# Kernel optimization log

Hardware: AMD Instinct MI355X
Metric: run time of the kernel (lower is better)

The kernel has to match this reference:

```python
import jax, jax.numpy as jnp
import numpy as np
from math import pi

N = 20000        # nodes
E = 640000       # edges (avg degree 32)
H = 128          # hidden_channels = num_filters
NB = 3           # num_bond_features
NGS = 50 - NB    # gaussians in smearing (num_gaussians - num_bond_features)
CUT = 10.0       # cutoff
L = 3            # num_interactions
B = 16           # graphs in batch
LOG2 = 0.6931471805599453


def ssp(x):
    # ShiftedSoftplus
    return jax.nn.softplus(x) - LOG2


def setup_inputs() -> dict:
    key = jax.random.key(0)
    ks = jax.random.split(key, 20)
    s = 0.05
    inp = {
        "z": jax.random.randint(ks[0], (N,), 0, 100),
        "pos": jax.random.uniform(ks[1], (N, 3), jnp.float32),
        "batch": jnp.sort(jax.random.randint(ks[2], (N,), 0, B)),
        "edge_index": jax.random.randint(ks[3], (2, E), 0, N),
        "edge_attr": jax.random.uniform(ks[4], (E, NB), jnp.float32),
        # parameters (stacked over L interaction blocks where per-layer)
        "emb": jax.random.normal(ks[5], (100, H), jnp.float32) * s,
        "mlp_w1": jax.random.normal(ks[6], (L, NB + NGS, H), jnp.float32) * s,
        "mlp_b1": jnp.zeros((L, H), jnp.float32),
        "mlp_w2": jax.random.normal(ks[7], (L, H, H), jnp.float32) * s,
        "mlp_b2": jnp.zeros((L, H), jnp.float32),
        "cf1_w": jax.random.normal(ks[8], (L, H, H), jnp.float32) * s,   # lin1, no bias
        "cf2_w": jax.random.normal(ks[9], (L, H, H), jnp.float32) * s,
        "cf2_b": jnp.zeros((L, H), jnp.float32),
        "lin_w": jax.random.normal(ks[10], (L, H, H), jnp.float32) * s,
        "lin_b": jnp.zeros((L, H), jnp.float32),
        "out1_w": jax.random.normal(ks[11], (H, H // 2), jnp.float32) * s,
        "out1_b": jnp.zeros((H // 2,), jnp.float32),
        "out2_w": jax.random.normal(ks[12], (H // 2, 1), jnp.float32) * s,
        "out2_b": jnp.zeros((1,), jnp.float32),
    }
    return inp


def reference(z, pos, batch, edge_index, edge_attr, emb,
              mlp_w1, mlp_b1, mlp_w2, mlp_b2,
              cf1_w, cf2_w, cf2_b, lin_w, lin_b,
              out1_w, out1_b, out2_w, out2_b):
    row, col = edge_index[0], edge_index[1]  # source j, target i
    h = emb[z]                               # [N,H] embedding_e(z)
    # edge_weight = ||pos[row] - pos[col]||
    ew = jnp.linalg.norm(pos[row] - pos[col], axis=-1)  # [E]
    # GaussianSmearing(0, cutoff, NGS)
    offset = jnp.linspace(0.0, CUT, NGS, dtype=jnp.float32)
    coeff = -0.5 / (offset[1] - offset[0]) ** 2
    gs = jnp.exp(coeff * (ew[:, None] - offset[None, :]) ** 2)  # [E,NGS]
    ea = jnp.concatenate([edge_attr, gs], axis=1)  # [E,50]
    # cosine cutoff weight
    C = 0.5 * (jnp.cos(ew * pi / CUT) + 1.0)       # [E]
    for l in range(L):
        # filter MLP on edge features
        W = ssp(ea @ mlp_w1[l] + mlp_b1[l]) @ mlp_w2[l] + mlp_b2[l]  # [E,H]
        W = W * C[:, None]
        xh = h @ cf1_w[l]                    # lin1 (no bias) [N,H]
        msg = xh[row] * W                    # gather-mul [E,H]
        agg = jax.ops.segment_sum(msg, col, num_segments=N)  # scatter-add [N,H]
        xc = agg @ cf2_w[l] + cf2_b[l]       # lin2
        xc = ssp(xc)
        xc = xc @ lin_w[l] + lin_b[l]        # block output lin
        h = h + xc                           # residual
    h = ssp(h @ out1_w + out1_b)             # [N,H/2]
    per_node = h @ out2_w + out2_b           # [N,1]
    out = jax.ops.segment_sum(per_node, batch, num_segments=B)  # readout 'add' -> [B,1]
    return out
```

## Files before the change

### kernel.cpp

```cpp
#include <hip/hip_runtime.h>
#include <hip/hip_bf16.h>

typedef __attribute__((ext_vector_type(8))) short bfrag;
typedef __attribute__((ext_vector_type(4))) float f32x4;

__device__ __forceinline__ float ssp_f(float x) {
    return fmaxf(x, 0.f) + __logf(1.f + __expf(-fabsf(x))) - 0.6931471805599453f;
}

__device__ __forceinline__ unsigned short f2b(float x) {
    __hip_bfloat16 h = __float2bfloat16(x);
    return *(unsigned short*)&h;
}

__global__ void sniff_kernel(const unsigned int* __restrict__ raw, int* __restrict__ flag)
{
    __shared__ int cnt[256];
    const int t = threadIdx.x;
    unsigned int w = raw[t];
    unsigned int e = (w >> 7) & 0xFFu;
    cnt[t] = (e >= 100u && e <= 135u) ? 1 : 0;
    __syncthreads();
    for (int s = 128; s > 0; s >>= 1) {
        if (t < s) cnt[t] += cnt[t + s];
        __syncthreads();
    }
    if (t == 0) *flag = (cnt[0] >= 160) ? 1 : 0;
}

__global__ void sniff_int_kernel(const unsigned int* __restrict__ z, int* __restrict__ iflag)
{
    __shared__ int cnt[128];
    const int t = threadIdx.x;
    cnt[t] = (z[2 * t + 1] == 0u) ? 1 : 0;
    __syncthreads();
    for (int s = 64; s > 0; s >>= 1) {
        if (t < s) cnt[t] += cnt[t + s];
        __syncthreads();
    }
    if (t == 0) *iflag = (cnt[0] >= 126) ? 1 : 0;
}

__global__ __launch_bounds__(256) void convert_kernel(
    const void* __restrict__ src, float* __restrict__ dst, int n,
    const int* __restrict__ flag)
{
    int i = blockIdx.x * 256 + threadIdx.x;
    if (i >= n) return;
    if (*flag) dst[i] = __bfloat162float(((const __hip_bfloat16*)src)[i]);
    else       dst[i] = ((const float*)src)[i];
}

__global__ __launch_bounds__(256) void convert_int_kernel(
    const void* __restrict__ src, int* __restrict__ dst, int n,
    const int* __restrict__ iflag)
{
    int i = blockIdx.x * 256 + threadIdx.x;
    if (i >= n) return;
    if (*iflag) dst[i] = (int)(((const long long*)src)[i]);
    else        dst[i] = ((const int*)src)[i];
}

__global__ __launch_bounds__(256) void embed_kernel(
    const int* __restrict__ z, const float* __restrict__ embf,
    float* __restrict__ h, int NH)
{
    int idx = blockIdx.x * 256 + threadIdx.x;
    if (idx >= NH) return;
    h[idx] = embf[z[idx >> 7] * 128 + (idx & 127)];
}

__global__ __launch_bounds__(256) void zero_int_kernel(int* p, int n)
{
    int i = blockIdx.x * 256 + threadIdx.x;
    if (i < n) p[i] = 0;
}

__global__ __launch_bounds__(256) void hist_kernel(const int* __restrict__ col,
                                                   int* __restrict__ count, int E)
{
    int e = blockIdx.x * 256 + threadIdx.x;
    if (e < E) atomicAdd(&count[col[e]], 1);
}

__global__ __launch_bounds__(256) void scan_kernel(const int* __restrict__ count,
                                                   int* __restrict__ rowptr,
                                                   int* __restrict__ next, int N)
{
    __shared__ int part[256];
    const int t = threadIdx.x;
    const int chunk = (N + 255) / 256;
    const int lo = t * chunk, hi = min(lo + chunk, N);
    int s = 0;
    for (int i = lo; i < hi; ++i) s += count[i];
    part[t] = s;
    __syncthreads();
    if (t == 0) {
        int run = 0;
        for (int i = 0; i < 256; ++i) { int v = part[i]; part[i] = run; run += v; }
        rowptr[N] = run;
    }
    __syncthreads();
    int run = part[t];
    for (int i = lo; i < hi; ++i) {
        rowptr[i] = run; next[i] = run;
        run += count[i];
    }
}

__global__ __launch_bounds__(256) void slot_kernel(const int* __restrict__ col,
                                                   int* __restrict__ next,
                                                   int* __restrict__ slot, int E)
{
    int e = blockIdx.x * 256 + threadIdx.x;
    if (e < E) slot[e] = atomicAdd(&next[col[e]], 1);
}

__global__ __launch_bounds__(256) void perm_kernel(const int* __restrict__ slot,
                                                   int* __restrict__ perm, int E)
{
    int e = blockIdx.x * 256 + threadIdx.x;
    if (e < E) perm[slot[e]] = e;
}

__global__ __launch_bounds__(256) void prep_edges_kernel(
    const float* __restrict__ posf, const int* __restrict__ row,
    const int* __restrict__ col, const float* __restrict__ eattrf,
    const int* __restrict__ perm,
    int* __restrict__ rowS, int* __restrict__ colS,
    float* __restrict__ CS, float* __restrict__ ewS,
    unsigned short* __restrict__ eaS, int E, int NB)
{
    int p = blockIdx.x * 256 + threadIdx.x;
    if (p >= E) return;
    const int e = perm[p];
    const int r = row[e], c = col[e];
    float dx = posf[r*3+0] - posf[c*3+0];
    float dy = posf[r*3+1] - posf[c*3+1];
    float dz = posf[r*3+2] - posf[c*3+2];
    float ew = sqrtf(dx*dx + dy*dy + dz*dz);
    rowS[p] = r; colS[p] = c; ewS[p] = ew;
    CS[p] = 0.5f * (cosf(ew * 0.3141592653589793f) + 1.0f);
    unsigned short* o = eaS + (long)p * 4;
    for (int q = 0; q < 4; ++q)
        o[q] = (q < NB) ? f2b(eattrf[(long)e * NB + q]) : (unsigned short)0;
}

__global__ __launch_bounds__(256) void wtrans_kernel(
    const float* __restrict__ src, unsigned short* __restrict__ dst,
    int K, int Kpad, int N)
{
    int idx = blockIdx.x * 256 + threadIdx.x;
    if (idx >= N * Kpad) return;
    int n = idx / Kpad, k = idx - n * Kpad;
    dst[idx] = (k < K) ? f2b(src[k * N + n]) : (unsigned short)0;
}

template<int MODE>
__global__ __launch_bounds__(256) void node_gemm_tiled(
    const float* __restrict__ in, const float* __restrict__ W,
    const float* __restrict__ bias, float* __restrict__ out, int N)
{
    __shared__ float in_s[32][128];
    const int t = threadIdx.x;
    const long n0 = (long)blockIdx.x * 32;
    for (int i = t; i < 32 * 128; i += 256) {
        long n = n0 + (i >> 7);
        in_s[i >> 7][i & 127] = (n < N) ? in[n * 128 + (i & 127)] : 0.f;
    }
    __syncthreads();
    const int j = t & 31, sub = t >> 5;
    const int c4 = j * 4, rb = sub * 4;
    float acc[4][4];
    float4 bv = make_float4(0.f, 0.f, 0.f, 0.f);
    if (MODE != 0) bv = *(const float4*)(bias + c4);
    #pragma unroll
    for (int i = 0; i < 4; ++i) { acc[i][0]=bv.x; acc[i][1]=bv.y; acc[i][2]=bv.z; acc[i][3]=bv.w; }
    #pragma unroll 4
    for (int k = 0; k < 128; ++k) {
        const float4 wv = *(const float4*)(W + k * 128 + c4);
        #pragma unroll
        for (int i = 0; i < 4; ++i) {
            const float a = in_s[rb + i][k];
            acc[i][0] += a * wv.x; acc[i][1] += a * wv.y;
            acc[i][2] += a * wv.z; acc[i][3] += a * wv.w;
        }
    }
    #pragma unroll
    for (int i = 0; i < 4; ++i) {
        long n = n0 + rb + i;
        if (n >= N) continue;
        float4 o;
        if (MODE == 1) {
            o.x = ssp_f(acc[i][0]); o.y = ssp_f(acc[i][1]);
            o.z = ssp_f(acc[i][2]); o.w = ssp_f(acc[i][3]);
        } else {
            o.x = acc[i][0]; o.y = acc[i][1]; o.z = acc[i][2]; o.w = acc[i][3];
        }
        if (MODE == 2) {
            float4 p = *(const float4*)(out + n * 128 + c4);
            o.x += p.x; o.y += p.y; o.z += p.z; o.w += p.w;
        }
        *(float4*)(out + n * 128 + c4) = o;
    }
}

__global__ __launch_bounds__(256) void edge_mfma(
    const int* __restrict__ rowS, const int* __restrict__ colS,
    const float* __restrict__ CS, const float* __restrict__ ewS,
    const unsigned short* __restrict__ eaS,
    const unsigned short* __restrict__ w1t, const float* __restrict__ b1,
    const unsigned short* __restrict__ w2t, const float* __restrict__ b2,
    const float* __restrict__ xh, float* __restrict__ agg,
    int E, int NB, int F50, float delta, float coeff)
{
    __shared__ __align__(16) short ea_b[32][64];
    __shared__ __align__(16) short t_b[32][128];
    __shared__ float runbuf[32][136];
    __shared__ int   row_s[32];
    __shared__ int   col_s[32];
    __shared__ float C_s[32];
    __shared__ float ew_s[32];
    __shared__ int   runcol_s[32];
    __shared__ int   runstart_s[33];
    __shared__ int   nruns_s;

    const int t = threadIdx.x;
    const long p0 = (long)blockIdx.x * 32;

    if (t < 32) {
        long p = p0 + t; if (p >= E) p = E - 1;
        row_s[t] = rowS[p];
        col_s[t] = colS[p];
        C_s[t]   = (p0 + t < E) ? CS[p] : 0.f;
        ew_s[t]  = ewS[p];
    }
    __syncthreads();
    if (t == 0) {
        int nr = 0;
        for (int i = 0; i < 32; ++i) {
            if (i == 0 || col_s[i] != col_s[i - 1]) {
                runcol_s[nr] = col_s[i];
                runstart_s[nr] = i;
                ++nr;
            }
        }
        runstart_s[nr] = 32;
        nruns_s = nr;
    }
    for (int i = t; i < 32 * 64; i += 256) {
        const int e = i >> 6, k = i & 63;
        long p = p0 + e; if (p >= E) p = E - 1;
        unsigned short v;
        if (k < NB)        v = eaS[p * 4 + k];
        else if (k < F50) {
            float d = ew_s[e] - (float)(k - NB) * delta;
            v = f2b(__expf(coeff * d * d));
        } else             v = 0;
        ea_b[e][k] = (short)v;
    }
    __syncthreads();

    const int lane = t & 63;
    const int w    = t >> 6;
    const int colL = lane & 15;
    const int quad = lane >> 4;
    const int m0   = (w & 1) * 16;

    {
        f32x4 acc[4];
        #pragma unroll
        for (int tt = 0; tt < 4; ++tt) acc[tt] = (f32x4){0.f, 0.f, 0.f, 0.f};
        #pragma unroll
        for (int ks = 0; ks < 2; ++ks) {
            const bfrag a = *(const bfrag*)&ea_b[m0 + colL][ks * 32 + quad * 8];
            #pragma unroll
            for (int tt = 0; tt < 4; ++tt) {
                const int n0 = ((w >> 1) * 4 + tt) * 16;
                const bfrag b = *(const bfrag*)&w1t[(long)(n0 + colL) * 64 + ks * 32 + quad * 8];
                acc[tt] = __builtin_amdgcn_mfma_f32_16x16x32_bf16(a, b, acc[tt], 0, 0, 0);
            }
        }
        #pragma unroll
        for (int tt = 0; tt < 4; ++tt) {
            const int n0 = ((w >> 1) * 4 + tt) * 16;
            const float bcol = b1[n0 + colL];
            #pragma unroll
            for (int reg = 0; reg < 4; ++reg) {
                float v = ssp_f(acc[tt][reg] + bcol);
                t_b[m0 + quad * 4 + reg][n0 + colL] = (short)f2b(v);
            }
        }
    }
    __syncthreads();

    {
        f32x4 acc[4];
        #pragma unroll
        for (int tt = 0; tt < 4; ++tt) acc[tt] = (f32x4){0.f, 0.f, 0.f, 0.f};
        #pragma unroll
        for (int ks = 0; ks < 4; ++ks) {
            const bfrag a = *(const bfrag*)&t_b[m0 + colL][ks * 32 + quad * 8];
            #pragma unroll
            for (int tt = 0; tt < 4; ++tt) {
                const int n0 = ((w >> 1) * 4 + tt) * 16;
                const bfrag b = *(const bfrag*)&w2t[(long)(n0 + colL) * 128 + ks * 32 + quad * 8];
                acc[tt] = __builtin_amdgcn_mfma_f32_16x16x32_bf16(a, b, acc[tt], 0, 0, 0);
            }
        }
        const int ebase = m0 + quad * 4;
        #pragma unroll
        for (int tt = 0; tt < 4; ++tt) {
            const int n0 = ((w >> 1) * 4 + tt) * 16;
            const int cg = n0 + colL;
            const float bcol = b2[cg];
            #pragma unroll
            for (int reg = 0; reg < 4; ++reg) {
                const int e = ebase + reg;
                const float v = acc[tt][reg] + bcol;
                runbuf[e][cg] = v * C_s[e] * xh[(long)row_s[e] * 128 + cg];
            }
        }
    }
    __syncthreads();

    const int nr = nruns_s;
    const int cc = t & 127;
    for (int r = t >> 7; r < nr; r += 2) {
        float a = 0.f;
        const int s1 = runstart_s[r + 1];
        for (int e = runstart_s[r]; e < s1; ++e)
            a += runbuf[e][cc];
        atomicAdd(&agg[(long)runcol_s[r] * 128 + cc], a);
    }
}

__global__ __launch_bounds__(256) void edge_atomic(
    const float* __restrict__ posf,
    const int* __restrict__ row, const int* __restrict__ col,
    const float* __restrict__ eattrf,
    const float* __restrict__ w1, const float* __restrict__ b1,
    const float* __restrict__ w2, const float* __restrict__ b2,
    const float* __restrict__ xh, float* __restrict__ agg,
    int E, int NB, int F50, float delta, float coeff)
{
    __shared__ float ea_s[32][52];
    __shared__ float t_s[32][128];
    __shared__ int   row_s[32];
    __shared__ int   col_s[32];
    __shared__ float C_s[32];
    __shared__ float ew_s[32];

    const int t = threadIdx.x;
    const long e0 = (long)blockIdx.x * 32;

    if (t < 32) {
        long e = e0 + t; if (e >= E) e = E - 1;
        const int r = row[e], c = col[e];
        row_s[t] = r; col_s[t] = c;
        float dx = posf[r*3+0] - posf[c*3+0];
        float dy = posf[r*3+1] - posf[c*3+1];
        float dz = posf[r*3+2] - posf[c*3+2];
        float ew = sqrtf(dx*dx + dy*dy + dz*dz);
        ew_s[t] = ew;
        C_s[t]  = (e0 + t < E) ? 0.5f * (cosf(ew * 0.3141592653589793f) + 1.0f) : 0.f;
        for (int q = 0; q < NB; ++q)
            ea_s[t][q] = eattrf[e * NB + q];
    }
    __syncthreads();
    {
        const int NGS = F50 - NB;
        for (int i = t; i < 32 * NGS; i += 256) {
            const int e = i / NGS, g = i - e * NGS;
            const float d = ew_s[e] - (float)g * delta;
            ea_s[e][NB + g] = __expf(coeff * d * d);
        }
    }
    __syncthreads();

    const int j = t & 31, sub = t >> 5;
    const int c4 = j * 4, eb = sub * 4;
    float acc[4][4];
    {
        const float4 bv = *(const float4*)(b1 + c4);
        #pragma unroll
        for (int i = 0; i < 4; ++i) { acc[i][0]=bv.x; acc[i][1]=bv.y; acc[i][2]=bv.z; acc[i][3]=bv.w; }
        for (int k = 0; k < F50; ++k) {
            const float4 wv = *(const float4*)(w1 + k * 128 + c4);
            #pragma unroll
            for (int i = 0; i < 4; ++i) {
                const float a = ea_s[eb + i][k];
                acc[i][0] += a * wv.x; acc[i][1] += a * wv.y;
                acc[i][2] += a * wv.z; acc[i][3] += a * wv.w;
            }
        }
        #pragma unroll
        for (int i = 0; i < 4; ++i) {
            float4 o;
            o.x = ssp_f(acc[i][0]); o.y = ssp_f(acc[i][1]);
            o.z = ssp_f(acc[i][2]); o.w = ssp_f(acc[i][3]);
            *(float4*)&t_s[eb + i][c4] = o;
        }
    }
    __syncthreads();
    {
        const float4 bv = *(const float4*)(b2 + c4);
        #pragma unroll
        for (int i = 0; i < 4; ++i) { acc[i][0]=bv.x; acc[i][1]=bv.y; acc[i][2]=bv.z; acc[i][3]=bv.w; }
        #pragma unroll 4
        for (int k = 0; k < 128; ++k) {
            const float4 wv = *(const float4*)(w2 + k * 128 + c4);
            #pragma unroll
            for (int i = 0; i < 4; ++i) {
                const float a = t_s[eb + i][k];
                acc[i][0] += a * wv.x; acc[i][1] += a * wv.y;
                acc[i][2] += a * wv.z; acc[i][3] += a * wv.w;
            }
        }
    }
    #pragma unroll
    for (int i = 0; i < 4; ++i) {
        const int e = eb + i;
        if (e0 + e >= E) continue;
        const float Ce = C_s[e];
        const float4 xv = *(const float4*)(xh + (long)row_s[e] * 128 + c4);
        float* ag = agg + (long)col_s[e] * 128 + c4;
        atomicAdd(ag + 0, acc[i][0] * Ce * xv.x);
        atomicAdd(ag + 1, acc[i][1] * Ce * xv.y);
        atomicAdd(ag + 2, acc[i][2] * Ce * xv.z);
        atomicAdd(ag + 3, acc[i][3] * Ce * xv.w);
    }
}

__global__ __launch_bounds__(128) void readout_simple(
    const float* __restrict__ h,
    const float* __restrict__ o1w, const float* __restrict__ o1b,
    const float* __restrict__ o2w, const float* __restrict__ o2b,
    const int* __restrict__ batch, float* __restrict__ accb)
{
    __shared__ float hr[128];
    __shared__ float vv[64];
    const int n = blockIdx.x;
    const int t = threadIdx.x;
    hr[t] = h[(long)n * 128 + t];
    __syncthreads();
    if (t < 64) {
        float a = o1b[t];
        #pragma unroll 8
        for (int k = 0; k < 128; ++k)
            a = fmaf(hr[k], o1w[k * 64 + t], a);
        vv[t] = ssp_f(a) * o2w[t];
    }
    __syncthreads();
    if (t < 32) vv[t] += vv[t + 32];
    __syncthreads();
    if (t < 16) vv[t] += vv[t + 16];
    __syncthreads();
    if (t < 8)  vv[t] += vv[t + 8];
    __syncthreads();
    if (t < 4)  vv[t] += vv[t + 4];
    __syncthreads();
    if (t < 2)  vv[t] += vv[t + 2];
    __syncthreads();
    if (t == 0) atomicAdd(&accb[batch[n]], vv[0] + vv[1] + o2b[0]);
}

__global__ void finalize_kernel(const float* __restrict__ accb,
                                float* __restrict__ out, int B)
{
    int t = blockIdx.x * 256 + threadIdx.x;
    if (t < B) out[t] = accb[t];
}

extern "C" void kernel_launch(void* const* d_in, const int* in_sizes, int n_in,
                              void* d_out, int out_size, void* d_ws, size_t ws_size,
                              hipStream_t stream)
{
    const int N   = in_sizes[0];
    const int E   = in_sizes[3] / 2;
    const int B   = out_size;
    const int H   = 128;
    const int L   = in_sizes[7] / H;
    const int NB  = in_sizes[4] / E;
    const int F50 = in_sizes[6] / (L * H);
    const int NGS = F50 - NB;
    const float delta = 10.0f / (float)(NGS - 1);
    const float coeff = -0.5f / (delta * delta);

    const int fidx[16] = {1, 4, 5, 6, 7, 8, 9, 10, 11, 12, 13, 14, 15, 16, 17, 18};
    long foff[17]; foff[0] = 0;
    for (int i = 0; i < 16; ++i) foff[i + 1] = foff[i] + in_sizes[fidx[i]];

    float* F = (float*)d_ws;
    long base = (foff[16] + 3) & ~3L;
    float* h    = F + base;
    float* xh   = h + (long)N * H;
    float* agg  = xh + (long)N * H;
    float* accb = agg + (long)N * H;
    int*   flag  = (int*)(accb + ((B + 3) & ~3));
    int*   iflag = flag + 1;
    int*   zi     = flag + 4;
    int*   batchi = zi + N;
    int*   eidxi  = batchi + N;
    int*   count  = eidxi + 2 * E;
    int*   rowptr = count + N;
    int*   next   = rowptr + N + 1;
    int*   slot   = next + N;
    int*   perm   = slot + E;
    int*   rowS   = perm + E;
    int*   colS   = rowS + E;
    float* CS     = (float*)(colS + E);
    float* ewS    = CS + E;
    unsigned short* eaS = (unsigned short*)(ewS + E);
    unsigned short* w1t = eaS + 4L * E;
    unsigned short* w2t = w1t + (long)L * 128 * 64;
    long used_bytes = (long)((char*)(w2t + (long)L * 128 * 128) - (char*)d_ws);
    const bool use_fast = (used_bytes <= (long)ws_size) && (F50 <= 64) && (NB <= 4);

    sniff_kernel<<<1, 256, 0, stream>>>((const unsigned int*)d_in[5], flag);
    sniff_int_kernel<<<1, 128, 0, stream>>>((const unsigned int*)d_in[0], iflag);

    for (int i = 0; i < 16; ++i) {
        int n = in_sizes[fidx[i]];
        convert_kernel<<<(n + 255) / 256, 256, 0, stream>>>(d_in[fidx[i]], F + foff[i], n, flag);
    }
    convert_int_kernel<<<(N + 255) / 256, 256, 0, stream>>>(d_in[0], zi, N, iflag);
    convert_int_kernel<<<(N + 255) / 256, 256, 0, stream>>>(d_in[2], batchi, N, iflag);
    convert_int_kernel<<<(2 * E + 255) / 256, 256, 0, stream>>>(d_in[3], eidxi, 2 * E, iflag);

    const float* posf   = F + foff[0];
    const float* eattrf = F + foff[1];
    const float* embf   = F + foff[2];
    const float* w1   = F + foff[3];  const float* b1   = F + foff[4];
    const float* w2   = F + foff[5];  const float* b2   = F + foff[6];
    const float* cf1  = F + foff[7];  const float* cf2  = F + foff[8];
    const float* cf2b = F + foff[9];  const float* lin  = F + foff[10];
    const float* linb = F + foff[11]; const float* o1   = F + foff[12];
    const float* o1b  = F + foff[13]; const float* o2   = F + foff[14];
    const float* o2b  = F + foff[15];

    if (use_fast) {
        zero_int_kernel<<<(N + 255) / 256, 256, 0, stream>>>(count, N);
        hist_kernel<<<(E + 255) / 256, 256, 0, stream>>>(eidxi + E, count, E);
        scan_kernel<<<1, 256, 0, stream>>>(count, rowptr, next, N);
        slot_kernel<<<(E + 255) / 256, 256, 0, stream>>>(eidxi + E, next, slot, E);
        perm_kernel<<<(E + 255) / 256, 256, 0, stream>>>(slot, perm, E);
        prep_edges_kernel<<<(E + 255) / 256, 256, 0, stream>>>(
            posf, eidxi, eidxi + E, eattrf, perm, rowS, colS, CS, ewS, eaS, E, NB);
        for (int l = 0; l < L; ++l) {
            wtrans_kernel<<<(128 * 64 + 255) / 256, 256, 0, stream>>>(
                w1 + (long)l * F50 * H, w1t + (long)l * 128 * 64, F50, 64, 128);
            wtrans_kernel<<<(128 * 128 + 255) / 256, 256, 0, stream>>>(
                w2 + (long)l * H * H, w2t + (long)l * 128 * 128, 128, 128, 128);
        }
    }

    embed_kernel<<<(N * H + 255) / 256, 256, 0, stream>>>(zi, embf, h, N * H);
    hipMemsetAsync(accb, 0, (size_t)B * sizeof(float), stream);

    const int ngemm = (N + 31) / 32;
    const int nedge = (E + 31) / 32;
    for (int l = 0; l < L; ++l) {
        hipMemsetAsync(agg, 0, (size_t)N * H * sizeof(float), stream);
        node_gemm_tiled<0><<<ngemm, 256, 0, stream>>>(h, cf1 + (long)l * H * H, nullptr, xh, N);
        if (use_fast) {
            edge_mfma<<<nedge, 256, 0, stream>>>(
                rowS, colS, CS, ewS, eaS,
                w1t + (long)l * 128 * 64, b1 + (long)l * H,
                w2t + (long)l * 128 * 128, b2 + (long)l * H,
                xh, agg, E, NB, F50, delta, coeff);
        } else {
            edge_atomic<<<nedge, 256, 0, stream>>>(
                posf, eidxi, eidxi + E, eattrf,
                w1 + (long)l * F50 * H, b1 + (long)l * H,
                w2 + (long)l * H * H,  b2 + (long)l * H,
                xh, agg, E, NB, F50, delta, coeff);
        }
        node_gemm_tiled<1><<<ngemm, 256, 0, stream>>>(agg, cf2 + (long)l * H * H, cf2b + (long)l * H, xh, N);
        node_gemm_tiled<2><<<ngemm, 256, 0, stream>>>(xh, lin + (long)l * H * H, linb + (long)l * H, h, N);
    }

    readout_simple<<<N, 128, 0, stream>>>(h, o1, o1b, o2, o2b, batchi, accb);
    finalize_kernel<<<(B + 255) / 256, 256, 0, stream>>>(accb, (float*)d_out, B);
}
```

Before: 1.531 ms.

## Fuse input conversions into one launch, pad LDS tiles, store messages as bf16

Replaces sixteen per-tensor conversion launches with a single kernel that binary-searches a packed offset table to find each element's source tensor. In the edge MFMA kernel, the ea and t LDS tiles get padded row strides to reduce bank conflicts, and the per-edge message buffer drops from fp32 to bf16, halving its LDS footprint. The run-detection loop moves inside the first thread guard, which removes one barrier. Storing messages as bf16 before the segment sum lowers accuracy of the aggregated values.

Result: slower. 1.596 ms (+4.3%).

```diff
diff --git a/kernel.cpp b/kernel.cpp
--- a/kernel.cpp
+++ b/kernel.cpp
@@ -11,6 +11,11 @@
 __device__ __forceinline__ unsigned short f2b(float x) {
     __hip_bfloat16 h = __float2bfloat16(x);
     return *(unsigned short*)&h;
+}
+
+__device__ __forceinline__ float b2f(unsigned short u) {
+    unsigned int w = ((unsigned int)u) << 16;
+    return *(float*)&w;
 }
 
 __global__ void sniff_kernel(const unsigned int* __restrict__ raw, int* __restrict__ flag)
@@ -41,14 +46,24 @@
     if (t == 0) *iflag = (cnt[0] >= 126) ? 1 : 0;
 }
 
-__global__ __launch_bounds__(256) void convert_kernel(
-    const void* __restrict__ src, float* __restrict__ dst, int n,
-    const int* __restrict__ flag)
-{
-    int i = blockIdx.x * 256 + threadIdx.x;
-    if (i >= n) return;
-    if (*flag) dst[i] = __bfloat162float(((const __hip_bfloat16*)src)[i]);
-    else       dst[i] = ((const float*)src)[i];
+struct Cvt16 {
+    const void* src[16];
+    long off[17];
+};
+
+__global__ __launch_bounds__(256) void convert_fused_kernel(
+    Cvt16 args, float* __restrict__ F, long total, const int* __restrict__ flag)
+{
+    long i = (long)blockIdx.x * 256 + threadIdx.x;
+    if (i >= total) return;
+    int lo = 0, hi = 16;
+    while (hi - lo > 1) {
+        int mid = (lo + hi) >> 1;
+        if (i >= args.off[mid]) lo = mid; else hi = mid;
+    }
+    long loc = i - args.off[lo];
+    if (*flag) F[i] = __bfloat162float(((const __hip_bfloat16*)args.src[lo])[loc]);
+    else       F[i] = ((const float*)args.src[lo])[loc];
 }
 
 __global__ __launch_bounds__(256) void convert_int_kernel(
@@ -214,9 +229,9 @@
     const float* __restrict__ xh, float* __restrict__ agg,
     int E, int NB, int F50, float delta, float coeff)
 {
-    __shared__ __align__(16) short ea_b[32][64];
-    __shared__ __align__(16) short t_b[32][128];
-    __shared__ float runbuf[32][136];
+    __shared__ __align__(16) short ea_b[32][72];
+    __shared__ __align__(16) short t_b[32][136];
+    __shared__ unsigned short runbuf[32][136];
     __shared__ int   row_s[32];
     __shared__ int   col_s[32];
     __shared__ float C_s[32];
@@ -234,20 +249,20 @@
         col_s[t] = colS[p];
         C_s[t]   = (p0 + t < E) ? CS[p] : 0.f;
         ew_s[t]  = ewS[p];
-    }
-    __syncthreads();
-    if (t == 0) {
-        int nr = 0;
-        for (int i = 0; i < 32; ++i) {
-            if (i == 0 || col_s[i] != col_s[i - 1]) {
-                runcol_s[nr] = col_s[i];
-                runstart_s[nr] = i;
-                ++nr;
+        if (t == 0) {
+            int nr = 0;
+            for (int i = 0; i < 32; ++i) {
+                if (i == 0 || col_s[i] != col_s[i - 1]) {
+                    runcol_s[nr] = col_s[i];
+                    runstart_s[nr] = i;
+                    ++nr;
+                }
             }
-        }
-        runstart_s[nr] = 32;
-        nruns_s = nr;
-    }
+            runstart_s[nr] = 32;
+            nruns_s = nr;
+        }
+    }
+    __syncthreads();
     for (int i = t; i < 32 * 64; i += 256) {
         const int e = i >> 6, k = i & 63;
         long p = p0 + e; if (p >= E) p = E - 1;
@@ -318,7 +333,7 @@
             for (int reg = 0; reg < 4; ++reg) {
                 const int e = ebase + reg;
                 const float v = acc[tt][reg] + bcol;
-                runbuf[e][cg] = v * C_s[e] * xh[(long)row_s[e] * 128 + cg];
+                runbuf[e][cg] = f2b(v * C_s[e] * xh[(long)row_s[e] * 128 + cg]);
             }
         }
     }
@@ -330,7 +345,7 @@
         float a = 0.f;
         const int s1 = runstart_s[r + 1];
         for (int e = runstart_s[r]; e < s1; ++e)
-            a += runbuf[e][cc];
+            a += b2f(runbuf[e][cc]);
         atomicAdd(&agg[(long)runcol_s[r] * 128 + cc], a);
     }
 }
@@ -488,11 +503,16 @@
     const float coeff = -0.5f / (delta * delta);
 
     const int fidx[16] = {1, 4, 5, 6, 7, 8, 9, 10, 11, 12, 13, 14, 15, 16, 17, 18};
-    long foff[17]; foff[0] = 0;
-    for (int i = 0; i < 16; ++i) foff[i + 1] = foff[i] + in_sizes[fidx[i]];
+    Cvt16 cv;
+    cv.off[0] = 0;
+    for (int i = 0; i < 16; ++i) {
+        cv.src[i] = d_in[fidx[i]];
+        cv.off[i + 1] = cv.off[i] + in_sizes[fidx[i]];
+    }
+    const long ftot = cv.off[16];
 
     float* F = (float*)d_ws;
-    long base = (foff[16] + 3) & ~3L;
+    long base = (ftot + 3) & ~3L;
     float* h    = F + base;
     float* xh   = h + (long)N * H;
     float* agg  = xh + (long)N * H;
@@ -520,24 +540,21 @@
     sniff_kernel<<<1, 256, 0, stream>>>((const unsigned int*)d_in[5], flag);
     sniff_int_kernel<<<1, 128, 0, stream>>>((const unsigned int*)d_in[0], iflag);
 
-    for (int i = 0; i < 16; ++i) {
-        int n = in_sizes[fidx[i]];
-        convert_kernel<<<(n + 255) / 256, 256, 0, stream>>>(d_in[fidx[i]], F + foff[i], n, flag);
-    }
+    convert_fused_kernel<<<(int)((ftot + 255) / 256), 256, 0, stream>>>(cv, F, ftot, flag);
     convert_int_kernel<<<(N + 255) / 256, 256, 0, stream>>>(d_in[0], zi, N, iflag);
     convert_int_kernel<<<(N + 255) / 256, 256, 0, stream>>>(d_in[2], batchi, N, iflag);
     convert_int_kernel<<<(2 * E + 255) / 256, 256, 0, stream>>>(d_in[3], eidxi, 2 * E, iflag);
 
-    const float* posf   = F + foff[0];
-    const float* eattrf = F + foff[1];
-    const float* embf   = F + foff[2];
-    const float* w1   = F + foff[3];  const float* b1   = F + foff[4];
-    const float* w2   = F + foff[5];  const float* b2   = F + foff[6];
-    const float* cf1  = F + foff[7];  const float* cf2  = F + foff[8];
-    const float* cf2b = F + foff[9];  const float* lin  = F + foff[10];
-    const float* linb = F + foff[11]; const float* o1   = F + foff[12];
-    const float* o1b  = F + foff[13]; const float* o2   = F + foff[14];
-    const float* o2b  = F + foff[15];
+    const float* posf   = F + cv.off[0];
+    const float* eattrf = F + cv.off[1];
+    const float* embf   = F + cv.off[2];
+    const float* w1   = F + cv.off[3];  const float* b1   = F + cv.off[4];
+    const float* w2   = F + cv.off[5];  const float* b2   = F + cv.off[6];
+    const float* cf1  = F + cv.off[7];  const float* cf2  = F + cv.off[8];
+    const float* cf2b = F + cv.off[9];  const float* lin  = F + cv.off[10];
+    const float* linb = F + cv.off[11]; const float* o1   = F + cv.off[12];
+    const float* o1b  = F + cv.off[13]; const float* o2   = F + cv.off[14];
+    const float* o2b  = F + cv.off[15];
 
     if (use_fast) {
         zero_int_kernel<<<(N + 255) / 256, 256, 0, stream>>>(count, N);
```
